# Kernel optimization log

Hardware: AMD Instinct MI355X
Metric: run time of the kernel (lower is better)

## Reference

```python
import math
import jax, jax.numpy as jnp
import numpy as np

B, S, OBS, ACT, D, H, F, L = 4, 512, 64, 16, 1024, 16, 4096, 4
T = 2 * S - 1  # 1023


def setup_inputs() -> dict:
    key = jax.random.key(0)
    ks = iter(jax.random.split(key, 48))
    def nrm(shape, scale=0.02):
        return (jax.random.normal(next(ks), shape, dtype=jnp.float32) * scale)
    z = lambda *s: jnp.zeros(s, jnp.float32)
    o = lambda *s: jnp.ones(s, jnp.float32)
    inp = {
        'observations': jax.random.normal(next(ks), (B, S, OBS), jnp.float32),
        'actions': jax.random.normal(next(ks), (B, S - 1, ACT), jnp.float32),
        # input_fc: obs_size -> D -> D -> D
        'in_w1': nrm((OBS, D)), 'in_b1': z(D), 'in_w2': nrm((D, D)), 'in_b2': z(D), 'in_w3': nrm((D, D)), 'in_b3': z(D),
        # action_fc: action_size -> D -> D -> D
        'act_w1': nrm((ACT, D)), 'act_b1': z(D), 'act_w2': nrm((D, D)), 'act_b2': z(D), 'act_w3': nrm((D, D)), 'act_b3': z(D),
        # output_fc: D -> D -> D -> action_size
        'out_w1': nrm((D, D)), 'out_b1': z(D), 'out_w2': nrm((D, D)), 'out_b2': z(D), 'out_w3': nrm((D, ACT)), 'out_b3': z(ACT),
        # decoder self-attn (stacked over L layers)
        'sa_w_in': nrm((L, D, 3 * D)), 'sa_b_in': z(L, 3 * D), 'sa_w_out': nrm((L, D, D)), 'sa_b_out': z(L, D),
        # decoder cross-attn
        'ca_w_in': nrm((L, D, 3 * D)), 'ca_b_in': z(L, 3 * D), 'ca_w_out': nrm((L, D, D)), 'ca_b_out': z(L, D),
        # decoder FFN
        'ff_w1': nrm((L, D, F)), 'ff_b1': z(L, F), 'ff_w2': nrm((L, F, D)), 'ff_b2': z(L, D),
        # layer norms
        'ln1_g': o(L, D), 'ln1_b': z(L, D), 'ln2_g': o(L, D), 'ln2_b': z(L, D), 'ln3_g': o(L, D), 'ln3_b': z(L, D),
        'lnf_g': o(D), 'lnf_b': z(D),
    }
    return inp


def _mlp(x, w1, b1, w2, b2, w3, b3):
    x = jax.nn.relu(x @ w1 + b1)
    x = jax.nn.relu(x @ w2 + b2)
    return x @ w3 + b3


def _ln(x, g, b, eps=1e-5):
    mu = x.mean(-1, keepdims=True)
    var = ((x - mu) ** 2).mean(-1, keepdims=True)
    return (x - mu) * jax.lax.rsqrt(var + eps) * g + b


def _mha(q_in, kv_in, w_in, b_in, w_out, b_out, mask):
    Bq, Tq, Dm = q_in.shape
    Tk = kv_in.shape[1]
    dh = Dm // H
    q = q_in @ w_in[:, :Dm] + b_in[:Dm]
    k = kv_in @ w_in[:, Dm:2 * Dm] + b_in[Dm:2 * Dm]
    v = kv_in @ w_in[:, 2 * Dm:] + b_in[2 * Dm:]
    q = q.reshape(Bq, Tq, H, dh).transpose(0, 2, 1, 3)
    k = k.reshape(Bq, Tk, H, dh).transpose(0, 2, 1, 3)
    v = v.reshape(Bq, Tk, H, dh).transpose(0, 2, 1, 3)
    s = jnp.einsum('bhqd,bhkd->bhqk', q, k) / math.sqrt(dh)
    if mask is not None:
        s = s + mask
    a = jax.nn.softmax(s, axis=-1)
    out = jnp.einsum('bhqk,bhkd->bhqd', a, v).transpose(0, 2, 1, 3).reshape(Bq, Tq, Dm)
    return out @ w_out + b_out


def reference(observations, actions,
              in_w1, in_b1, in_w2, in_b2, in_w3, in_b3,
              act_w1, act_b1, act_w2, act_b2, act_w3, act_b3,
              out_w1, out_b1, out_w2, out_b2, out_w3, out_b3,
              sa_w_in, sa_b_in, sa_w_out, sa_b_out,
              ca_w_in, ca_b_in, ca_w_out, ca_b_out,
              ff_w1, ff_b1, ff_w2, ff_b2,
              ln1_g, ln1_b, ln2_g, ln2_b, ln3_g, ln3_b, lnf_g, lnf_b):
    obs_tok = _mlp(observations, in_w1, in_b1, in_w2, in_b2, in_w3, in_b3)   # [B,S,D]
    act_tok = _mlp(actions, act_w1, act_b1, act_w2, act_b2, act_w3, act_b3)  # [B,S-1,D]
    # fused interleave [obs1, act1, obs2, ..., obsS] (replaces the python loops)
    tgt = jnp.zeros((B, T, D), obs_tok.dtype).at[:, 0::2].set(obs_tok).at[:, 1::2].set(act_tok)
    # PositionalEncoding is applied on a batch-first tensor in the original code,
    # so pe[:x.size(0)] indexes by BATCH and broadcasts over the sequence dim (bug-faithful).
    pos = jnp.arange(B, dtype=jnp.float32)[:, None]
    div = jnp.exp(jnp.arange(0, D, 2, dtype=jnp.float32) * (-math.log(10000.0) / D))
    pe = jnp.stack([jnp.sin(pos * div), jnp.cos(pos * div)], axis=-1).reshape(B, D)
    x = tgt + pe[:, None, :]
    mask = jnp.triu(jnp.full((T, T), -jnp.inf, dtype=jnp.float32), k=1)
    mem = jnp.zeros((B, 1, D), x.dtype)  # inp_tok (zero memory token)
    for l in range(L):  # post-norm nn.TransformerDecoderLayer, dropout=0
        x = _ln(x + _mha(x, x, sa_w_in[l], sa_b_in[l], sa_w_out[l], sa_b_out[l], mask), ln1_g[l], ln1_b[l])
        x = _ln(x + _mha(x, mem, ca_w_in[l], ca_b_in[l], ca_w_out[l], ca_b_out[l], None), ln2_g[l], ln2_b[l])
        ff = jax.nn.relu(x @ ff_w1[l] + ff_b1[l]) @ ff_w2[l] + ff_b2[l]
        x = _ln(x + ff, ln3_g[l], ln3_b[l])
    x = _ln(x, lnf_g, lnf_b)  # nn.Transformer final decoder norm
    return _mlp(x, out_w1, out_b1, out_w2, out_b2, out_w3, out_b3)  # [B,T,action_size]
```

## Files before the change

kernel.cpp:

```cpp
#include <hip/hip_runtime.h>
#include <hip/hip_bf16.h>
#include <cstdint>
#include <cstddef>

#define B_  4
#define S_  512
#define T_  1023
#define D_  1024
#define H_  16
#define DH_ 64
#define F_  4096
#define L_  4

typedef float f32x4 __attribute__((ext_vector_type(4)));
typedef __bf16 bf16x8 __attribute__((ext_vector_type(8)));

__device__ inline unsigned pack_bf2(float a, float b) {
    union { __hip_bfloat16 h; unsigned short u; } ua, ub;
    ua.h = __float2bfloat16(a); ub.h = __float2bfloat16(b);
    return (unsigned)ua.u | ((unsigned)ub.u << 16);
}

__global__ __launch_bounds__(256) void gemm_bf16(
    const __hip_bfloat16* __restrict__ A, const __hip_bfloat16* __restrict__ Wt,
    const float* __restrict__ bias,
    float* __restrict__ Cf, float* __restrict__ Cf2,
    __hip_bfloat16* __restrict__ Cb,
    int M, int K, int N, int relu, int ksplit)
{
    __shared__ __align__(16) __hip_bfloat16 AsmB[3][128 * 32];
    __shared__ __align__(16) __hip_bfloat16 BsmB[3][128 * 32];
    const int tid  = threadIdx.x;
    const int lane = tid & 63;
    const int w    = tid >> 6;
    const int wr   = w >> 1, wc = w & 1;
    const int l15  = lane & 15, l4 = lane >> 4;

    const int gx = gridDim.x;
    int bid = blockIdx.y * gx + blockIdx.x;
    {
        const int nwg = gx * gridDim.y;
        const int q = nwg >> 3, r = nwg & 7;
        const int xcd = bid & 7, idx = bid >> 3;
        bid = (xcd < r ? xcd * (q + 1) : r * (q + 1) + (xcd - r) * q) + idx;
    }
    const int row0 = (bid / gx) * 128;
    const int col0 = (bid % gx) * 128;
    const int z = blockIdx.z;
    const int kslice = K / ksplit;
    const int kbase = z * kslice;

    f32x4 acc[4][4] = {};

    auto stage = [&](__hip_bfloat16* As, __hip_bfloat16* Bs, int kt) {
        auto* ldsA = (__attribute__((address_space(3))) char*)As;
        auto* ldsB = (__attribute__((address_space(3))) char*)Bs;
        #pragma unroll
        for (int half = 0; half < 2; ++half) {
            const int ch = half * 256 + tid;
            const int r  = ch >> 2;
            const int c  = (ch & 3) * 8;
            int gr = row0 + r; gr = (gr < M) ? gr : (M - 1);
            const __hip_bfloat16* srcA = A + (size_t)gr * K + kt + c;
            __builtin_amdgcn_global_load_lds(
                (const __attribute__((address_space(1))) unsigned*)srcA,
                (__attribute__((address_space(3))) unsigned*)(ldsA + (size_t)ch * 16),
                16, 0, 0);
            int gc = col0 + r; gc = (gc < N) ? gc : (N - 1);
            const __hip_bfloat16* srcB = Wt + (size_t)gc * K + kt + c;
            __builtin_amdgcn_global_load_lds(
                (const __attribute__((address_space(1))) unsigned*)srcB,
                (__attribute__((address_space(3))) unsigned*)(ldsB + (size_t)ch * 16),
                16, 0, 0);
        }
    };
    auto compute = [&](const __hip_bfloat16* As, const __hip_bfloat16* Bs) {
        const __hip_bfloat16* ab = As + (size_t)(wr * 64 + l15) * 32 + l4 * 8;
        const __hip_bfloat16* bb = Bs + (size_t)(wc * 64 + l15) * 32 + l4 * 8;
        bf16x8 af[4], bf[4];
        #pragma unroll
        for (int mi = 0; mi < 4; ++mi) af[mi] = *(const bf16x8*)(ab + mi * 16 * 32);
        #pragma unroll
        for (int nj = 0; nj < 4; ++nj) bf[nj] = *(const bf16x8*)(bb + nj * 16 * 32);
        #pragma unroll
        for (int mi = 0; mi < 4; ++mi)
            #pragma unroll
            for (int nj = 0; nj < 4; ++nj)
                acc[mi][nj] = __builtin_amdgcn_mfma_f32_16x16x32_bf16(
                    af[mi], bf[nj], acc[mi][nj], 0, 0, 0);
    };

    const int nk = kslice >> 5;
    __hip_bfloat16 *A0 = AsmB[0], *A1 = AsmB[1], *A2 = AsmB[2];
    __hip_bfloat16 *B0 = BsmB[0], *B1 = BsmB[1], *B2 = BsmB[2];
    stage(A0, B0, kbase);
    if (nk > 1) stage(A1, B1, kbase + 32);
    for (int t = 0; t < nk; ++t) {
        if (t + 1 < nk) {
            asm volatile("s_waitcnt vmcnt(4)" ::: "memory");
        } else {
            asm volatile("s_waitcnt vmcnt(0)" ::: "memory");
        }
        __builtin_amdgcn_s_barrier();
        if (t + 2 < nk) stage(A2, B2, kbase + (t + 2) * 32);
        compute(A0, B0);
        __hip_bfloat16* ta = A0; A0 = A1; A1 = A2; A2 = ta;
        __hip_bfloat16* tb = B0; B0 = B1; B1 = B2; B2 = tb;
    }

    if (ksplit > 1) {
        const size_t MN = (size_t)M * N;
        float* dst = (z < 2) ? (Cf + (size_t)z * MN) : (Cf2 + (size_t)(z - 2) * MN);
        #pragma unroll
        for (int nj = 0; nj < 4; ++nj) {
            const int c = col0 + wc * 64 + nj * 16 + l15;
            if (c >= N) continue;
            #pragma unroll
            for (int mi = 0; mi < 4; ++mi)
                #pragma unroll
                for (int i = 0; i < 4; ++i) {
                    const int r = row0 + wr * 64 + mi * 16 + l4 * 4 + i;
                    if (r < M) dst[(size_t)r * N + c] = acc[mi][nj][i];
                }
        }
    } else {
        #pragma unroll
        for (int nj = 0; nj < 4; ++nj) {
            const int c = col0 + wc * 64 + nj * 16 + l15;
            if (c >= N) continue;
            const float bv = bias[c];
            #pragma unroll
            for (int mi = 0; mi < 4; ++mi)
                #pragma unroll
                for (int i = 0; i < 4; ++i) {
                    const int r = row0 + wr * 64 + mi * 16 + l4 * 4 + i;
                    if (r >= M) continue;
                    float v = acc[mi][nj][i] + bv;
                    if (relu) v = fmaxf(v, 0.f);
                    if (Cf) Cf[(size_t)r * N + c] = v;
                    if (Cb) Cb[(size_t)r * N + c] = __float2bfloat16(v);
                }
        }
    }
}

__global__ __launch_bounds__(256) void reduce_split(
    const float* __restrict__ part, const float* __restrict__ part2,
    int SK, size_t pstride,
    const float* __restrict__ bias, int N, int total4, int relu,
    float* __restrict__ outf, __hip_bfloat16* __restrict__ outb)
{
    const int idx4 = blockIdx.x * 256 + threadIdx.x;
    if (idx4 >= total4) return;
    const size_t base = (size_t)idx4 * 4;
    const int c = (int)(base & (size_t)(N - 1));
    float4 v = *(const float4*)(part + base);
    for (int s = 1; s < SK; ++s) {
        const float* src = (s < 2) ? (part + (size_t)s * pstride)
                                   : (part2 + (size_t)(s - 2) * pstride);
        const float4 p = *(const float4*)(src + base);
        v.x += p.x; v.y += p.y; v.z += p.z; v.w += p.w;
    }
    const float4 bv = *(const float4*)(bias + c);
    v.x += bv.x; v.y += bv.y; v.z += bv.z; v.w += bv.w;
    if (relu) {
        v.x = fmaxf(v.x, 0.f); v.y = fmaxf(v.y, 0.f);
        v.z = fmaxf(v.z, 0.f); v.w = fmaxf(v.w, 0.f);
    }
    if (outf) *(float4*)(outf + base) = v;
    if (outb) {
        __hip_bfloat16* o = outb + base;
        o[0] = __float2bfloat16(v.x); o[1] = __float2bfloat16(v.y);
        o[2] = __float2bfloat16(v.z); o[3] = __float2bfloat16(v.w);
    }
}

__global__ __launch_bounds__(256) void transpose_w(
    const float* __restrict__ W, __hip_bfloat16* __restrict__ Wt,
    int K, int N, int Kpad)
{
    __shared__ float t[32][33];
    W  += (size_t)blockIdx.z * K * N;
    Wt += (size_t)blockIdx.z * N * Kpad;
    const int n0 = blockIdx.x * 32, k0 = blockIdx.y * 32;
    const int tx = threadIdx.x & 31, ty = threadIdx.x >> 5;
    #pragma unroll
    for (int i = 0; i < 4; ++i) {
        int r = ty + i * 8;
        int k = k0 + r, n = n0 + tx;
        t[r][tx] = (k < K && n < N) ? W[(size_t)k * N + n] : 0.f;
    }
    __syncthreads();
    #pragma unroll
    for (int i = 0; i < 4; ++i) {
        int r = ty + i * 8;
        int n = n0 + r, k = k0 + tx;
        if (n < N && k < Kpad) Wt[(size_t)n * Kpad + k] = __float2bfloat16(t[tx][r]);
    }
}

__global__ __launch_bounds__(256) void convert_pad(
    const float* __restrict__ in, __hip_bfloat16* __restrict__ out,
    int M, int Kin, int Kout)
{
    int idx = blockIdx.x * 256 + threadIdx.x;
    if (idx >= M * Kout) return;
    int r = idx / Kout, c = idx - r * Kout;
    out[idx] = __float2bfloat16(c < Kin ? in[(size_t)r * Kin + c] : 0.f);
}

__global__ __launch_bounds__(256) void v_transpose(
    const __hip_bfloat16* __restrict__ qkvb, __hip_bfloat16* __restrict__ vt)
{
    __shared__ __hip_bfloat16 tile[32][33];
    const int b  = blockIdx.z;
    const int c0 = blockIdx.x * 32;
    const int t0 = blockIdx.y * 32;
    const int tx = threadIdx.x & 31, ty = threadIdx.x >> 5;
    const __hip_bfloat16 z = __float2bfloat16(0.f);
    #pragma unroll
    for (int i = 0; i < 4; ++i) {
        const int tl = ty + i * 8;
        const int t = t0 + tl;
        tile[tl][tx] = (t < T_) ? qkvb[(size_t)(b * T_ + t) * 3072 + 2048 + c0 + tx] : z;
    }
    __syncthreads();
    #pragma unroll
    for (int i = 0; i < 4; ++i) {
        const int cl = ty + i * 8;
        const int t = t0 + tx;
        vt[((size_t)(b * 1024 + c0 + cl)) * 1024 + t] = (t < T_) ? tile[tx][cl] : z;
    }
}

__global__ __launch_bounds__(256) void attn_mfma(
    const __hip_bfloat16* __restrict__ qkvb,
    const __hip_bfloat16* __restrict__ vt,
    __hip_bfloat16* __restrict__ out)
{
    __shared__ __align__(16) __hip_bfloat16 Qs[2][128][32];
    __shared__ __align__(16) __hip_bfloat16 Ks[2][64][32];
    __shared__ __align__(16) __hip_bfloat16 Vs[2][64][32];
    __shared__ __align__(16) __hip_bfloat16 Ps[4][2][32][32];
    __shared__ float Lw[4][2][16];

    const int bh = blockIdx.x;
    const int b = bh >> 4, h = bh & 15;
    const int q0 = blockIdx.y * 128;
    const int tid = threadIdx.x;
    const int w = tid >> 6, lane = tid & 63;
    const int l15 = lane & 15, l4 = lane >> 4;
    const size_t ldq = 3 * D_;

    {
        #pragma unroll
        for (int c = 0; c < 2; ++c)
            #pragma unroll
            for (int it = 0; it < 2; ++it) {
                const int ch = it * 256 + tid;
                const int r = ch >> 2, cp = ch & 3;
                int qr = q0 + r; qr = (qr < T_) ? qr : (T_ - 1);
                const __hip_bfloat16* src = qkvb + (size_t)(b * T_ + qr) * ldq + h * 64 + c * 32 + cp * 8;
                __builtin_amdgcn_global_load_lds(
                    (const __attribute__((address_space(1))) unsigned*)src,
                    (__attribute__((address_space(3))) unsigned*)((__attribute__((address_space(3))) char*)&Qs[c][0][0] + ch * 16),
                    16, 0, 0);
            }
    }
    __syncthreads();
    bf16x8 qreg[2][2];
    #pragma unroll
    for (int qf = 0; qf < 2; ++qf)
        #pragma unroll
        for (int c = 0; c < 2; ++c)
            qreg[qf][c] = *(const bf16x8*)&Qs[c][w * 32 + qf * 16 + l15][l4 * 8];

    f32x4 of[2][4] = {};
    float lp[2] = {0.f, 0.f};
    const int qmaxw = q0 + w * 32 + 31;
    const int kend = (q0 + 128 < T_) ? (q0 + 128) : T_;

    for (int k0 = 0; k0 < kend; k0 += 64) {
        __syncthreads();
        {
            const int r = tid >> 2, cp = tid & 3;
            #pragma unroll
            for (int c = 0; c < 2; ++c) {
                int kr = k0 + r; kr = (kr < T_) ? kr : (T_ - 1);
                const __hip_bfloat16* srcK = qkvb + (size_t)(b * T_ + kr) * ldq + D_ + h * 64 + c * 32 + cp * 8;
                __builtin_amdgcn_global_load_lds(
                    (const __attribute__((address_space(1))) unsigned*)srcK,
                    (__attribute__((address_space(3))) unsigned*)((__attribute__((address_space(3))) char*)&Ks[c][0][0] + tid * 16),
                    16, 0, 0);
                const __hip_bfloat16* srcV = vt + ((size_t)(b * 1024 + h * 64 + r)) * 1024 + k0 + c * 32 + cp * 8;
                __builtin_amdgcn_global_load_lds(
                    (const __attribute__((address_space(1))) unsigned*)srcV,
                    (__attribute__((address_space(3))) unsigned*)((__attribute__((address_space(3))) char*)&Vs[c][0][0] + tid * 16),
                    16, 0, 0);
            }
        }
        __syncthreads();

        if (k0 <= qmaxw) {
            f32x4 sf[4][2] = {};
            #pragma unroll
            for (int c = 0; c < 2; ++c) {
                bf16x8 kf[4];
                #pragma unroll
                for (int kfr = 0; kfr < 4; ++kfr)
                    kf[kfr] = *(const bf16x8*)&Ks[c][kfr * 16 + l15][l4 * 8];
                #pragma unroll
                for (int kfr = 0; kfr < 4; ++kfr)
                    #pragma unroll
                    for (int qf = 0; qf < 2; ++qf)
                        sf[kfr][qf] = __builtin_amdgcn_mfma_f32_16x16x32_bf16(
                            kf[kfr], qreg[qf][c], sf[kfr][qf], 0, 0, 0);
            }
            const bool needmask = (k0 + 63) > (q0 + w * 32);
            #pragma unroll
            for (int kfr = 0; kfr < 4; ++kfr) {
                #pragma unroll
                for (int qf = 0; qf < 2; ++qf) {
                    const int qg = q0 + w * 32 + qf * 16 + l15;
                    float p[4];
                    #pragma unroll
                    for (int i = 0; i < 4; ++i) {
                        const int kg = k0 + kfr * 16 + l4 * 4 + i;
                        float pv = __expf(sf[kfr][qf][i] * 0.125f);
                        if (needmask && kg > qg) pv = 0.f;
                        p[i] = pv;
                        lp[qf] += pv;
                    }
                    unsigned* dst = (unsigned*)&Ps[w][kfr >> 1][qf * 16 + l15][(kfr & 1) * 16 + l4 * 4];
                    dst[0] = pack_bf2(p[0], p[1]);
                    dst[1] = pack_bf2(p[2], p[3]);
                }
            }
            #pragma unroll
            for (int kc = 0; kc < 2; ++kc) {
                bf16x8 pa[2], vb[4];
                #pragma unroll
                for (int qf = 0; qf < 2; ++qf)
                    pa[qf] = *(const bf16x8*)&Ps[w][kc][qf * 16 + l15][l4 * 8];
                #pragma unroll
                for (int df = 0; df < 4; ++df)
                    vb[df] = *(const bf16x8*)&Vs[kc][df * 16 + l15][l4 * 8];
                #pragma unroll
                for (int qf = 0; qf < 2; ++qf)
                    #pragma unroll
                    for (int df = 0; df < 4; ++df)
                        of[qf][df] = __builtin_amdgcn_mfma_f32_16x16x32_bf16(
                            pa[qf], vb[df], of[qf][df], 0, 0, 0);
            }
        }
    }

    #pragma unroll
    for (int qf = 0; qf < 2; ++qf) {
        float v = lp[qf];
        v += __shfl_xor(v, 16);
        v += __shfl_xor(v, 32);
        if (l4 == 0) Lw[w][qf][l15] = v;
    }
    __syncthreads();
    #pragma unroll
    for (int qf = 0; qf < 2; ++qf) {
        float inv[4];
        #pragma unroll
        for (int i = 0; i < 4; ++i) inv[i] = 1.f / Lw[w][qf][l4 * 4 + i];
        #pragma unroll
        for (int df = 0; df < 4; ++df) {
            #pragma unroll
            for (int i = 0; i < 4; ++i) {
                const int qg = q0 + w * 32 + qf * 16 + l4 * 4 + i;
                if (qg < T_)
                    out[(size_t)(b * T_ + qg) * D_ + h * 64 + df * 16 + l15] =
                        __float2bfloat16(of[qf][df][i] * inv[i]);
            }
        }
    }
}

__device__ inline void block_ln_stats(float4 v, float& mu, float& inv,
                                      float* ws, float* ws2, float* mu_s, float* inv_s)
{
    const int tid = threadIdx.x;
    float s  = v.x + v.y + v.z + v.w;
    float s2 = v.x * v.x + v.y * v.y + v.z * v.z + v.w * v.w;
    #pragma unroll
    for (int off = 32; off; off >>= 1) {
        s  += __shfl_down(s, off);
        s2 += __shfl_down(s2, off);
    }
    const int wid = tid >> 6;
    if ((tid & 63) == 0) { ws[wid] = s; ws2[wid] = s2; }
    __syncthreads();
    if (tid == 0) {
        float S  = ws[0] + ws[1] + ws[2] + ws[3];
        float S2 = ws2[0] + ws2[1] + ws2[2] + ws2[3];
        float m = S * (1.f / (float)D_);
        float var = S2 * (1.f / (float)D_) - m * m;
        *mu_s = m;
        *inv_s = rsqrtf(var + 1e-5f);
    }
    __syncthreads();
    mu = *mu_s; inv = *inv_s;
}

__global__ __launch_bounds__(256) void add_ln_kernel(
    float* __restrict__ x, const float* __restrict__ p, const float* __restrict__ p2,
    int SK, size_t pstride, const float* __restrict__ pbias,
    const float* __restrict__ g, const float* __restrict__ beta,
    __hip_bfloat16* __restrict__ xb)
{
    const int row = blockIdx.x;
    const int tid = threadIdx.x;
    __shared__ float ws[4], ws2[4], mu_s, inv_s;
    float4* xr = reinterpret_cast<float4*>(x + (size_t)row * D_);
    float4 v = xr[tid];
    if (p) {
        for (int s = 0; s < SK; ++s) {
            const float* src = (s < 2) ? (p + (size_t)s * pstride)
                                       : (p2 + (size_t)(s - 2) * pstride);
            const float4 wv = reinterpret_cast<const float4*>(src + (size_t)row * D_)[tid];
            v.x += wv.x; v.y += wv.y; v.z += wv.z; v.w += wv.w;
        }
        if (pbias) {
            const float4 bv = reinterpret_cast<const float4*>(pbias)[tid];
            v.x += bv.x; v.y += bv.y; v.z += bv.z; v.w += bv.w;
        }
    }
    float mu, inv;
    block_ln_stats(v, mu, inv, ws, ws2, &mu_s, &inv_s);
    const float4 gg = reinterpret_cast<const float4*>(g)[tid];
    const float4 bb = reinterpret_cast<const float4*>(beta)[tid];
    float4 o;
    o.x = (v.x - mu) * inv * gg.x + bb.x;
    o.y = (v.y - mu) * inv * gg.y + bb.y;
    o.z = (v.z - mu) * inv * gg.z + bb.z;
    o.w = (v.w - mu) * inv * gg.w + bb.w;
    xr[tid] = o;
    if (xb) {
        __hip_bfloat16* xo = xb + (size_t)row * D_ + tid * 4;
        xo[0] = __float2bfloat16(o.x);
        xo[1] = __float2bfloat16(o.y);
        xo[2] = __float2bfloat16(o.z);
        xo[3] = __float2bfloat16(o.w);
    }
}

__global__ __launch_bounds__(256) void add_ln2_kernel(
    float* __restrict__ x, const float* __restrict__ p, int SK, size_t pstride,
    const float* __restrict__ pbias, const float* __restrict__ cav,
    const float* __restrict__ g1, const float* __restrict__ b1,
    const float* __restrict__ g2, const float* __restrict__ b2,
    __hip_bfloat16* __restrict__ xb)
{
    const int row = blockIdx.x;
    const int tid = threadIdx.x;
    __shared__ float ws[4], ws2[4], mu_s, inv_s;
    float4* xr = reinterpret_cast<float4*>(x + (size_t)row * D_);
    float4 v = xr[tid];
    for (int s = 0; s < SK; ++s) {
        const float4 wv = reinterpret_cast<const float4*>(
            p + (size_t)s * pstride + (size_t)row * D_)[tid];
        v.x += wv.x; v.y += wv.y; v.z += wv.z; v.w += wv.w;
    }
    if (pbias) {
        const float4 bv = reinterpret_cast<const float4*>(pbias)[tid];
        v.x += bv.x; v.y += bv.y; v.z += bv.z; v.w += bv.w;
    }
    float mu, inv;
    block_ln_stats(v, mu, inv, ws, ws2, &mu_s, &inv_s);
    const float4 g1v = reinterpret_cast<const float4*>(g1)[tid];
    const float4 b1v = reinterpret_cast<const float4*>(b1)[tid];
    const float4 cv  = reinterpret_cast<const float4*>(cav)[tid];
    float4 u;
    u.x = (v.x - mu) * inv * g1v.x + b1v.x + cv.x;
    u.y = (v.y - mu) * inv * g1v.y + b1v.y + cv.y;
    u.z = (v.z - mu) * inv * g1v.z + b1v.z + cv.z;
    u.w = (v.w - mu) * inv * g1v.w + b1v.w + cv.w;
    __syncthreads();
    float mu2, inv2;
    block_ln_stats(u, mu2, inv2, ws, ws2, &mu_s, &inv_s);
    const float4 g2v = reinterpret_cast<const float4*>(g2)[tid];
    const float4 b2v = reinterpret_cast<const float4*>(b2)[tid];
    float4 o;
    o.x = (u.x - mu2) * inv2 * g2v.x + b2v.x;
    o.y = (u.y - mu2) * inv2 * g2v.y + b2v.y;
    o.z = (u.z - mu2) * inv2 * g2v.z + b2v.z;
    o.w = (u.w - mu2) * inv2 * g2v.w + b2v.w;
    xr[tid] = o;
    __hip_bfloat16* xo = xb + (size_t)row * D_ + tid * 4;
    xo[0] = __float2bfloat16(o.x);
    xo[1] = __float2bfloat16(o.y);
    xo[2] = __float2bfloat16(o.z);
    xo[3] = __float2bfloat16(o.w);
}

__global__ __launch_bounds__(256) void interleave_pe_kernel(
    const float* __restrict__ obs_tok, const float* __restrict__ act_tok,
    float* __restrict__ x, __hip_bfloat16* __restrict__ xb)
{
    const int row = blockIdx.x;
    const int b = row / T_;
    const int t = row - b * T_;
    const float* src = (t & 1)
        ? (act_tok + (size_t)(b * (S_ - 1) + (t >> 1)) * D_)
        : (obs_tok + (size_t)(b * S_ + (t >> 1)) * D_);
    float* xr = x + (size_t)row * D_;
    __hip_bfloat16* xo = xb + (size_t)row * D_;
    #pragma unroll
    for (int k = 0; k < 4; ++k) {
        int d = threadIdx.x + k * 256;
        float ang = (float)b * expf(-(float)(d & ~1) * (9.210340371976184f / 1024.0f));
        float pe = (d & 1) ? cosf(ang) : sinf(ang);
        float v = src[d] + pe;
        xr[d] = v;
        xo[d] = __float2bfloat16(v);
    }
}

__global__ __launch_bounds__(256) void ca_part_kernel(
    const float* __restrict__ ca_b_in, const float* __restrict__ ca_w_out,
    float* __restrict__ part)
{
    const int idx = blockIdx.x * 256 + threadIdx.x;
    const int ks = blockIdx.y;
    const int l = idx >> 10, d = idx & 1023;
    const float* bv = ca_b_in + (size_t)l * 3 * D_ + 2 * D_ + ks * 64;
    const float* wp = ca_w_out + (size_t)l * D_ * D_ + (size_t)(ks * 64) * D_ + d;
    float s = 0.f;
    #pragma unroll 8
    for (int k = 0; k < 64; ++k) s = fmaf(bv[k], wp[(size_t)k * D_], s);
    part[(size_t)ks * (L_ * D_) + idx] = s;
}

__global__ __launch_bounds__(256) void ca_reduce_kernel(
    const float* __restrict__ part, const float* __restrict__ ca_b_out,
    float* __restrict__ out)
{
    const int idx = blockIdx.x * 256 + threadIdx.x;
    float s = ca_b_out[idx];
    #pragma unroll
    for (int ks = 0; ks < 16; ++ks) s += part[(size_t)ks * (L_ * D_) + idx];
    out[idx] = s;
}

extern "C" void kernel_launch(void* const* d_in, const int* in_sizes, int n_in,
                              void* d_out, int out_size, void* d_ws, size_t ws_size,
                              hipStream_t stream)
{
    const float* obs     = (const float*)d_in[0];
    const float* act     = (const float*)d_in[1];
    const float* in_w1   = (const float*)d_in[2];
    const float* in_b1   = (const float*)d_in[3];
    const float* in_w2   = (const float*)d_in[4];
    const float* in_b2   = (const float*)d_in[5];
    const float* in_w3   = (const float*)d_in[6];
    const float* in_b3   = (const float*)d_in[7];
    const float* act_w1  = (const float*)d_in[8];
    const float* act_b1  = (const float*)d_in[9];
    const float* act_w2  = (const float*)d_in[10];
    const float* act_b2  = (const float*)d_in[11];
    const float* act_w3  = (const float*)d_in[12];
    const float* act_b3  = (const float*)d_in[13];
    const float* out_w1  = (const float*)d_in[14];
    const float* out_b1  = (const float*)d_in[15];
    const float* out_w2  = (const float*)d_in[16];
    const float* out_b2  = (const float*)d_in[17];
    const float* out_w3  = (const float*)d_in[18];
    const float* out_b3  = (const float*)d_in[19];
    const float* sa_w_in = (const float*)d_in[20];
    const float* sa_b_in = (const float*)d_in[21];
    const float* sa_w_out= (const float*)d_in[22];
    const float* sa_b_out= (const float*)d_in[23];
    const float* ca_b_in = (const float*)d_in[25];
    const float* ca_w_out= (const float*)d_in[26];
    const float* ca_b_out= (const float*)d_in[27];
    const float* ff_w1   = (const float*)d_in[28];
    const float* ff_b1   = (const float*)d_in[29];
    const float* ff_w2   = (const float*)d_in[30];
    const float* ff_b2   = (const float*)d_in[31];
    const float* ln1_g   = (const float*)d_in[32];
    const float* ln1_b   = (const float*)d_in[33];
    const float* ln2_g   = (const float*)d_in[34];
    const float* ln2_b   = (const float*)d_in[35];
    const float* ln3_g   = (const float*)d_in[36];
    const float* ln3_b   = (const float*)d_in[37];
    const float* lnf_g   = (const float*)d_in[38];
    const float* lnf_b   = (const float*)d_in[39];

    const int MT = B_ * T_;
    const int Mo = B_ * S_;
    const int Ma = B_ * (S_ - 1);

    char* base = (char*)d_ws;
    size_t used = 0;
    auto alloc = [&](size_t bytes) -> char* {
        char* r = base + used;
        used += (bytes + 255) & ~(size_t)255;
        return r;
    };
    typedef __hip_bfloat16 bf;
    bf* wi1  = (bf*)alloc((size_t)1024 * 64 * 2);
    bf* wi2  = (bf*)alloc((size_t)1024 * 1024 * 2);
    bf* wi3  = (bf*)alloc((size_t)1024 * 1024 * 2);
    bf* wa1  = (bf*)alloc((size_t)1024 * 32 * 2);
    bf* wa2  = (bf*)alloc((size_t)1024 * 1024 * 2);
    bf* wa3  = (bf*)alloc((size_t)1024 * 1024 * 2);
    bf* wo1  = (bf*)alloc((size_t)1024 * 1024 * 2);
    bf* wo2  = (bf*)alloc((size_t)1024 * 1024 * 2);
    bf* wo3  = (bf*)alloc((size_t)16 * 1024 * 2);
    bf* wsin = (bf*)alloc((size_t)L_ * 3072 * 1024 * 2);
    bf* wsout= (bf*)alloc((size_t)L_ * 1024 * 1024 * 2);
    bf* wf1  = (bf*)alloc((size_t)L_ * 4096 * 1024 * 2);
    bf* wf2  = (bf*)alloc((size_t)L_ * 1024 * 4096 * 2);
    bf* obs_bf = (bf*)alloc((size_t)Mo * 64 * 2);
    bf* act_bf = (bf*)alloc((size_t)Ma * 32 * 2);
    bf* x_bf   = (bf*)alloc((size_t)MT * D_ * 2);
    bf* attnb  = (bf*)alloc((size_t)MT * D_ * 2);
    bf* h1b    = (bf*)alloc((size_t)MT * D_ * 2);
    bf* h2b    = (bf*)alloc((size_t)MT * D_ * 2);
    char* shared_rg = alloc((size_t)MT * F_ * 2);
    bf* qkvb = (bf*)shared_rg;
    bf* ffh  = (bf*)shared_rg;
    bf* vt   = (bf*)alloc((size_t)B_ * 1024 * 1024 * 2);
    float* x       = (float*)alloc((size_t)MT * D_ * 4);
    float* y       = (float*)alloc((size_t)MT * D_ * 4);
    float* obs_tok = (float*)alloc((size_t)Mo * D_ * 4);
    float* act_tok = (float*)alloc((size_t)Ma * D_ * 4);
    float* ca      = (float*)alloc((size_t)L_ * D_ * 4);
    float* ca_part = (float*)alloc((size_t)16 * L_ * D_ * 4);
    if (used > ws_size) return;
    float* part_loop = y;
    float* part_pre  = (float*)shared_rg;
    float* part_post = (float*)shared_rg;
    float* part_extra = (float*)(base + used);
    const size_t extra_bytes = (size_t)2 * MT * D_ * 4;
    const int ES4 = (used + extra_bytes <= ws_size) ? 1 : 0;

    auto tw = [&](const float* W, bf* Wt, int K, int N, int Kpad, int batch) {
        dim3 g((N + 31) / 32, (Kpad + 31) / 32, batch);
        transpose_w<<<g, 256, 0, stream>>>(W, Wt, K, N, Kpad);
    };
    auto gemm = [&](const bf* A, const bf* Wt, const float* bias,
                    float* Cf, float* Cf2, bf* Cb,
                    int M, int K, int N, int relu, int sk) {
        dim3 g((N + 127) / 128, (M + 127) / 128, sk);
        gemm_bf16<<<g, 256, 0, stream>>>(A, Wt, bias, Cf, Cf2, Cb, M, K, N, relu, sk);
    };
    auto gemm_red = [&](const bf* A, const bf* Wt, const float* bias,
                        float* Cf, bf* Cb, int M, int K, int N, int relu, int sk,
                        float* part) {
        if (sk <= 1) { gemm(A, Wt, bias, Cf, nullptr, Cb, M, K, N, relu, 1); return; }
        const size_t MN = (size_t)M * N;
        gemm(A, Wt, nullptr, part, part + 2 * MN, nullptr, M, K, N, 0, sk);
        const int total4 = (int)(MN / 4);
        reduce_split<<<(total4 + 255) / 256, 256, 0, stream>>>(
            part, part + 2 * MN, sk, MN, bias, N, total4, relu, Cf, Cb);
    };

    tw(in_w1,  wi1, 64,   1024, 64,   1);
    tw(in_w2,  wi2, 1024, 1024, 1024, 1);
    tw(in_w3,  wi3, 1024, 1024, 1024, 1);
    tw(act_w1, wa1, 16,   1024, 32,   1);
    tw(act_w2, wa2, 1024, 1024, 1024, 1);
    tw(act_w3, wa3, 1024, 1024, 1024, 1);
    tw(out_w1, wo1, 1024, 1024, 1024, 1);
    tw(out_w2, wo2, 1024, 1024, 1024, 1);
    tw(out_w3, wo3, 1024, 16,   1024, 1);
    tw(sa_w_in,  wsin,  1024, 3072, 1024, L_);
    tw(sa_w_out, wsout, 1024, 1024, 1024, L_);
    tw(ff_w1,    wf1,   1024, 4096, 1024, L_);
    tw(ff_w2,    wf2,   4096, 1024, 4096, L_);

    convert_pad<<<(Mo * 64 + 255) / 256, 256, 0, stream>>>(obs, obs_bf, Mo, 64, 64);
    convert_pad<<<(Ma * 32 + 255) / 256, 256, 0, stream>>>(act, act_bf, Ma, 16, 32);
    ca_part_kernel<<<dim3((L_ * D_) / 256, 16), 256, 0, stream>>>(ca_b_in, ca_w_out, ca_part);
    ca_reduce_kernel<<<(L_ * D_) / 256, 256, 0, stream>>>(ca_part, ca_b_out, ca);

    gemm(obs_bf, wi1, in_b1, nullptr, nullptr, h1b, Mo, 64, D_, 1, 1);
    gemm_red(h1b, wi2, in_b2, nullptr, h2b, Mo, D_, D_, 1, 4, part_pre);
    gemm_red(h2b, wi3, in_b3, obs_tok, nullptr, Mo, D_, D_, 0, 4, part_pre);
    gemm(act_bf, wa1, act_b1, nullptr, nullptr, h1b, Ma, 32, D_, 1, 1);
    gemm_red(h1b, wa2, act_b2, nullptr, h2b, Ma, D_, D_, 1, 4, part_pre);
    gemm_red(h2b, wa3, act_b3, act_tok, nullptr, Ma, D_, D_, 0, 4, part_pre);

    interleave_pe_kernel<<<MT, 256, 0, stream>>>(obs_tok, act_tok, x, x_bf);

    for (int l = 0; l < L_; ++l) {
        gemm(x_bf, wsin + (size_t)l * 3072 * 1024, sa_b_in + (size_t)l * 3 * D_,
             nullptr, nullptr, qkvb, MT, D_, 3 * D_, 0, 1);
        v_transpose<<<dim3(32, 32, B_), 256, 0, stream>>>(qkvb, vt);
        attn_mfma<<<dim3(B_ * H_, 8), 256, 0, stream>>>(qkvb, vt, attnb);
        gemm(attnb, wsout + (size_t)l * 1024 * 1024, nullptr,
             part_loop, nullptr, nullptr, MT, D_, D_, 0, 2);
        add_ln2_kernel<<<MT, 256, 0, stream>>>(x, part_loop, 2, (size_t)MT * D_,
             sa_b_out + (size_t)l * D_, ca + (size_t)l * D_,
             ln1_g + (size_t)l * D_, ln1_b + (size_t)l * D_,
             ln2_g + (size_t)l * D_, ln2_b + (size_t)l * D_, x_bf);
        gemm(x_bf, wf1 + (size_t)l * 4096 * 1024, ff_b1 + (size_t)l * F_,
             nullptr, nullptr, ffh, MT, D_, F_, 1, 1);
        if (ES4) {
            gemm(ffh, wf2 + (size_t)l * 1024 * 4096, nullptr,
                 part_loop, part_extra, nullptr, MT, F_, D_, 0, 4);
            add_ln_kernel<<<MT, 256, 0, stream>>>(x, part_loop, part_extra, 4,
                 (size_t)MT * D_, ff_b2 + (size_t)l * D_,
                 ln3_g + (size_t)l * D_, ln3_b + (size_t)l * D_, x_bf);
        } else {
            gemm(ffh, wf2 + (size_t)l * 1024 * 4096, nullptr,
                 part_loop, nullptr, nullptr, MT, F_, D_, 0, 2);
            add_ln_kernel<<<MT, 256, 0, stream>>>(x, part_loop, part_loop, 2,
                 (size_t)MT * D_, ff_b2 + (size_t)l * D_,
                 ln3_g + (size_t)l * D_, ln3_b + (size_t)l * D_, x_bf);
        }
    }

    add_ln_kernel<<<MT, 256, 0, stream>>>(x, nullptr, nullptr, 0, 0, nullptr,
                                          lnf_g, lnf_b, x_bf);
    gemm_red(x_bf, wo1, out_b1, nullptr, h1b, MT, D_, D_, 1, 2, part_post);
    gemm_red(h1b,  wo2, out_b2, nullptr, h2b, MT, D_, D_, 1, 2, part_post);
    gemm_red(h2b,  wo3, out_b3, (float*)d_out, nullptr, MT, D_, 16, 0, 8, part_post);
}
```

Before: 1.486 ms.

## Fuse V transpose into QKV GEMM epilogue and shrink GEMM N-tile

The QKV projection GEMM now writes the V columns directly in transposed layout from its epilogue, so the separate v_transpose kernel launch and its extra read and write of V go away. Every GEMM also moves from 128x128 to 128x64 output tiles, which halves the B-operand LDS staging and the accumulator registers and doubles the number of workgroups. In exchange, each tile reuses loaded data less, and the transposed epilogue stores are strided and poorly coalesced. The zero padding the old transpose wrote at the unused token position is no longer written.

```diff
diff --git a/kernel.cpp b/kernel.cpp
--- a/kernel.cpp
+++ b/kernel.cpp
@@ -26,10 +26,11 @@
     const float* __restrict__ bias,
     float* __restrict__ Cf, float* __restrict__ Cf2,
     __hip_bfloat16* __restrict__ Cb,
-    int M, int K, int N, int relu, int ksplit)
+    int M, int K, int N, int relu, int ksplit,
+    __hip_bfloat16* __restrict__ vtp, int vtw)
 {
     __shared__ __align__(16) __hip_bfloat16 AsmB[3][128 * 32];
-    __shared__ __align__(16) __hip_bfloat16 BsmB[3][128 * 32];
+    __shared__ __align__(16) __hip_bfloat16 BsmB[3][64 * 32];
     const int tid  = threadIdx.x;
     const int lane = tid & 63;
     const int w    = tid >> 6;
@@ -45,12 +46,12 @@
         bid = (xcd < r ? xcd * (q + 1) : r * (q + 1) + (xcd - r) * q) + idx;
     }
     const int row0 = (bid / gx) * 128;
-    const int col0 = (bid % gx) * 128;
+    const int col0 = (bid % gx) * 64;
     const int z = blockIdx.z;
     const int kslice = K / ksplit;
     const int kbase = z * kslice;
 
-    f32x4 acc[4][4] = {};
+    f32x4 acc[4][2] = {};
 
     auto stage = [&](__hip_bfloat16* As, __hip_bfloat16* Bs, int kt) {
         auto* ldsA = (__attribute__((address_space(3))) char*)As;
@@ -66,26 +67,30 @@
                 (const __attribute__((address_space(1))) unsigned*)srcA,
                 (__attribute__((address_space(3))) unsigned*)(ldsA + (size_t)ch * 16),
                 16, 0, 0);
+        }
+        {
+            const int r = tid >> 2;
+            const int c = (tid & 3) * 8;
             int gc = col0 + r; gc = (gc < N) ? gc : (N - 1);
             const __hip_bfloat16* srcB = Wt + (size_t)gc * K + kt + c;
             __builtin_amdgcn_global_load_lds(
                 (const __attribute__((address_space(1))) unsigned*)srcB,
-                (__attribute__((address_space(3))) unsigned*)(ldsB + (size_t)ch * 16),
+                (__attribute__((address_space(3))) unsigned*)(ldsB + (size_t)tid * 16),
                 16, 0, 0);
         }
     };
     auto compute = [&](const __hip_bfloat16* As, const __hip_bfloat16* Bs) {
         const __hip_bfloat16* ab = As + (size_t)(wr * 64 + l15) * 32 + l4 * 8;
-        const __hip_bfloat16* bb = Bs + (size_t)(wc * 64 + l15) * 32 + l4 * 8;
-        bf16x8 af[4], bf[4];
+        const __hip_bfloat16* bb = Bs + (size_t)(wc * 32 + l15) * 32 + l4 * 8;
+        bf16x8 af[4], bf[2];
         #pragma unroll
         for (int mi = 0; mi < 4; ++mi) af[mi] = *(const bf16x8*)(ab + mi * 16 * 32);
         #pragma unroll
-        for (int nj = 0; nj < 4; ++nj) bf[nj] = *(const bf16x8*)(bb + nj * 16 * 32);
+        for (int nj = 0; nj < 2; ++nj) bf[nj] = *(const bf16x8*)(bb + nj * 16 * 32);
         #pragma unroll
         for (int mi = 0; mi < 4; ++mi)
             #pragma unroll
-            for (int nj = 0; nj < 4; ++nj)
+            for (int nj = 0; nj < 2; ++nj)
                 acc[mi][nj] = __builtin_amdgcn_mfma_f32_16x16x32_bf16(
                     af[mi], bf[nj], acc[mi][nj], 0, 0, 0);
     };
@@ -97,7 +102,7 @@
     if (nk > 1) stage(A1, B1, kbase + 32);
     for (int t = 0; t < nk; ++t) {
         if (t + 1 < nk) {
-            asm volatile("s_waitcnt vmcnt(4)" ::: "memory");
+            asm volatile("s_waitcnt vmcnt(3)" ::: "memory");
         } else {
             asm volatile("s_waitcnt vmcnt(0)" ::: "memory");
         }
@@ -112,8 +117,8 @@
         const size_t MN = (size_t)M * N;
         float* dst = (z < 2) ? (Cf + (size_t)z * MN) : (Cf2 + (size_t)(z - 2) * MN);
         #pragma unroll
-        for (int nj = 0; nj < 4; ++nj) {
-            const int c = col0 + wc * 64 + nj * 16 + l15;
+        for (int nj = 0; nj < 2; ++nj) {
+            const int c = col0 + wc * 32 + nj * 16 + l15;
             if (c >= N) continue;
             #pragma unroll
             for (int mi = 0; mi < 4; ++mi)
@@ -123,10 +128,32 @@
                     if (r < M) dst[(size_t)r * N + c] = acc[mi][nj][i];
                 }
         }
+    } else if (vtw) {
+        #pragma unroll
+        for (int nj = 0; nj < 2; ++nj) {
+            const int c = col0 + wc * 32 + nj * 16 + l15;
+            const float bv = bias[c];
+            #pragma unroll
+            for (int mi = 0; mi < 4; ++mi)
+                #pragma unroll
+                for (int i = 0; i < 4; ++i) {
+                    const int r = row0 + wr * 64 + mi * 16 + l4 * 4 + i;
+                    if (r >= M) continue;
+                    const float v = acc[mi][nj][i] + bv;
+                    if (c < 2048) {
+                        Cb[(size_t)r * N + c] = __float2bfloat16(v);
+                    } else {
+                        const int b = r / T_;
+                        const int tl = r - b * T_;
+                        vtp[((size_t)(b * 1024 + (c - 2048))) * 1024 + tl] =
+                            __float2bfloat16(v);
+                    }
+                }
+        }
     } else {
         #pragma unroll
-        for (int nj = 0; nj < 4; ++nj) {
-            const int c = col0 + wc * 64 + nj * 16 + l15;
+        for (int nj = 0; nj < 2; ++nj) {
+            const int c = col0 + wc * 32 + nj * 16 + l15;
             if (c >= N) continue;
             const float bv = bias[c];
             #pragma unroll
@@ -207,30 +234,6 @@
     if (idx >= M * Kout) return;
     int r = idx / Kout, c = idx - r * Kout;
     out[idx] = __float2bfloat16(c < Kin ? in[(size_t)r * Kin + c] : 0.f);
-}
-
-__global__ __launch_bounds__(256) void v_transpose(
-    const __hip_bfloat16* __restrict__ qkvb, __hip_bfloat16* __restrict__ vt)
-{
-    __shared__ __hip_bfloat16 tile[32][33];
-    const int b  = blockIdx.z;
-    const int c0 = blockIdx.x * 32;
-    const int t0 = blockIdx.y * 32;
-    const int tx = threadIdx.x & 31, ty = threadIdx.x >> 5;
-    const __hip_bfloat16 z = __float2bfloat16(0.f);
-    #pragma unroll
-    for (int i = 0; i < 4; ++i) {
-        const int tl = ty + i * 8;
-        const int t = t0 + tl;
-        tile[tl][tx] = (t < T_) ? qkvb[(size_t)(b * T_ + t) * 3072 + 2048 + c0 + tx] : z;
-    }
-    __syncthreads();
-    #pragma unroll
-    for (int i = 0; i < 4; ++i) {
-        const int cl = ty + i * 8;
-        const int t = t0 + tx;
-        vt[((size_t)(b * 1024 + c0 + cl)) * 1024 + t] = (t < T_) ? tile[tx][cl] : z;
-    }
 }
 
 __global__ __launch_bounds__(256) void attn_mfma(
@@ -646,9 +649,11 @@
     };
     auto gemm = [&](const bf* A, const bf* Wt, const float* bias,
                     float* Cf, float* Cf2, bf* Cb,
-                    int M, int K, int N, int relu, int sk) {
-        dim3 g((N + 127) / 128, (M + 127) / 128, sk);
-        gemm_bf16<<<g, 256, 0, stream>>>(A, Wt, bias, Cf, Cf2, Cb, M, K, N, relu, sk);
+                    int M, int K, int N, int relu, int sk,
+                    bf* vtp = nullptr, int vtw = 0) {
+        dim3 g((N + 63) / 64, (M + 127) / 128, sk);
+        gemm_bf16<<<g, 256, 0, stream>>>(A, Wt, bias, Cf, Cf2, Cb,
+                                          M, K, N, relu, sk, vtp, vtw);
     };
     auto gemm_red = [&](const bf* A, const bf* Wt, const float* bias,
                         float* Cf, bf* Cb, int M, int K, int N, int relu, int sk,
@@ -691,8 +696,7 @@
 
     for (int l = 0; l < L_; ++l) {
         gemm(x_bf, wsin + (size_t)l * 3072 * 1024, sa_b_in + (size_t)l * 3 * D_,
-             nullptr, nullptr, qkvb, MT, D_, 3 * D_, 0, 1);
-        v_transpose<<<dim3(32, 32, B_), 256, 0, stream>>>(qkvb, vt);
+             nullptr, nullptr, qkvb, MT, D_, 3 * D_, 0, 1, vt, 1);
         attn_mfma<<<dim3(B_ * H_, 8), 256, 0, stream>>>(qkvb, vt, attnb);
         gemm(attnb, wsout + (size_t)l * 1024 * 1024, nullptr,
              part_loop, nullptr, nullptr, MT, D_, D_, 0, 2);
```

Result: no change. 1.478 ms (-0.5%).
